# Performance work log

Hardware: AMD Instinct MI355X
Metric: run time of the kernel (lower is better)

## Reference

```python
import jax, jax.numpy as jnp
import numpy as np

N_NODES = 100000
N_EDGES = 3200000
IN_F = 256
OUT_F = 128


def setup_inputs() -> dict:
    key = jax.random.key(0)
    k1, k2, k3, k4, k5, k6 = jax.random.split(key, 6)
    x = jax.random.normal(k1, (N_NODES, IN_F), dtype=jnp.float32)
    edge_row = jax.random.randint(k2, (N_EDGES,), 0, N_NODES, dtype=jnp.int32)
    edge_col = jax.random.randint(k3, (N_EDGES,), 0, N_NODES, dtype=jnp.int32)
    edge_val = jax.random.uniform(k4, (N_EDGES,), dtype=jnp.float32)
    stdv = 1.0 / np.sqrt(OUT_F)
    weight = jax.random.uniform(k5, (IN_F, OUT_F), dtype=jnp.float32, minval=-stdv, maxval=stdv)
    bias = jax.random.uniform(k6, (OUT_F,), dtype=jnp.float32, minval=-stdv, maxval=stdv)
    return {"x": x, "edge_row": edge_row, "edge_col": edge_col,
            "edge_val": edge_val, "weight": weight, "bias": bias}


def reference(x, edge_row, edge_col, edge_val, weight, bias):
    # dropout p=0.0 -> identity. support = x @ W  [N, out_f]
    support = x @ weight
    # spmm(adj, support): out[r] = sum_e adj_val[e] * support[col[e]] for edges with row[e]==r
    gathered = support[edge_col] * edge_val[:, None]  # [E, out_f]
    out = jax.ops.segment_sum(gathered, edge_row, num_segments=N_NODES)
    out = out + bias
    return jax.nn.relu(out)
```

## Files before the change

### kernel.cpp

```cpp
#include <hip/hip_runtime.h>
#include <hip/hip_fp16.h>

#define IN_F 256
#define OUT_F 128
#define RPB 128
#define LOG_RPB 7
#define MAXB 1024
#define CHUNK 8192

typedef __attribute__((ext_vector_type(8))) short short8;
typedef __attribute__((ext_vector_type(4))) float f32x4;

__device__ inline short bf16r(float f) {
  unsigned u = __float_as_uint(f);
  u += 0x7FFF + ((u >> 16) & 1);
  return (short)(u >> 16);
}

__global__ __launch_bounds__(512) void gemm_mfma(const float* __restrict__ x,
                                                 const float* __restrict__ w,
                                                 __half* __restrict__ sup,
                                                 int n_nodes) {
  __shared__ short wlds[128 * 256];
  int t = threadIdx.x;
  for (int idx = t; idx < 256 * 128; idx += 512) {
    int k = idx >> 7;
    int n = idx & 127;
    int g = k >> 3;
    wlds[n * 256 + ((g ^ (n & 7)) << 3) + (k & 7)] = bf16r(w[idx]);
  }
  __syncthreads();

  int lane = t & 63;
  int wid = t >> 6;
  int wrow = (wid >> 1) * 64;
  int wcol = (wid & 1) * 64;
  int row_blk = blockIdx.x * 256;

  int arow[4];
#pragma unroll
  for (int mt = 0; mt < 4; ++mt)
    arow[mt] = min(row_blk + wrow + mt * 16 + (lane & 15), n_nodes - 1);
  int koff = (lane >> 4) * 8;

  f32x4 acc[4][4];
#pragma unroll
  for (int mt = 0; mt < 4; ++mt)
#pragma unroll
    for (int nt = 0; nt < 4; ++nt) acc[mt][nt] = (f32x4){0.f, 0.f, 0.f, 0.f};

#pragma unroll 2
  for (int kk = 0; kk < IN_F; kk += 32) {
    short8 af[4];
#pragma unroll
    for (int mt = 0; mt < 4; ++mt) {
      const float* px = x + (size_t)arow[mt] * IN_F + kk + koff;
      float4 p = *(const float4*)px;
      float4 q = *(const float4*)(px + 4);
      short8 a;
      a[0] = bf16r(p.x); a[1] = bf16r(p.y); a[2] = bf16r(p.z); a[3] = bf16r(p.w);
      a[4] = bf16r(q.x); a[5] = bf16r(q.y); a[6] = bf16r(q.z); a[7] = bf16r(q.w);
      af[mt] = a;
    }
    short8 bf[4];
    int g = (kk >> 3) + (lane >> 4);
#pragma unroll
    for (int nt = 0; nt < 4; ++nt) {
      int n = wcol + nt * 16 + (lane & 15);
      bf[nt] = *(const short8*)&wlds[n * 256 + ((g ^ (n & 7)) << 3)];
    }
#pragma unroll
    for (int mt = 0; mt < 4; ++mt)
#pragma unroll
      for (int nt = 0; nt < 4; ++nt)
        acc[mt][nt] = __builtin_amdgcn_mfma_f32_16x16x32_bf16(af[mt], bf[nt],
                                                              acc[mt][nt], 0, 0, 0);
  }

#pragma unroll
  for (int mt = 0; mt < 4; ++mt)
#pragma unroll
    for (int nt = 0; nt < 4; ++nt)
#pragma unroll
      for (int reg = 0; reg < 4; ++reg) {
        int grow = row_blk + wrow + mt * 16 + (lane >> 4) * 4 + reg;
        int gcol = wcol + nt * 16 + (lane & 15);
        if (grow < n_nodes)
          sup[(size_t)grow * OUT_F + gcol] = __float2half(acc[mt][nt][reg]);
      }
}

__global__ __launch_bounds__(256) void hist2(const int* __restrict__ erow,
                                             int* __restrict__ cnt2d,
                                             int n_edges, int nbuck, int nblk) {
  __shared__ int h[MAXB];
  int t = threadIdx.x;
  for (int i = t; i < nbuck; i += 256) h[i] = 0;
  __syncthreads();
  int beg = blockIdx.x * CHUNK;
  int end = min(beg + CHUNK, n_edges);
  for (int e = beg + t; e < end; e += 256) atomicAdd(&h[erow[e] >> LOG_RPB], 1);
  __syncthreads();
  for (int i = t; i < nbuck; i += 256) cnt2d[(size_t)i * nblk + blockIdx.x] = h[i];
}

__global__ __launch_bounds__(256) void rowsum(const int* __restrict__ cnt2d,
                                              int* __restrict__ bcnt, int nblk) {
  __shared__ int red[256];
  int b = blockIdx.x;
  const int* row = cnt2d + (size_t)b * nblk;
  int t = threadIdx.x;
  int s = 0;
  for (int i = t; i < nblk; i += 256) s += row[i];
  red[t] = s;
  __syncthreads();
  for (int off = 128; off > 0; off >>= 1) {
    if (t < off) red[t] += red[t + off];
    __syncthreads();
  }
  if (t == 0) bcnt[b] = red[0];
}

__global__ __launch_bounds__(1024) void bucket_scan(const int* __restrict__ bcnt,
                                                    int* __restrict__ bptr, int nbuck) {
  __shared__ int sc[1024];
  int t = threadIdx.x;
  int v = (t < nbuck) ? bcnt[t] : 0;
  sc[t] = v;
  __syncthreads();
  for (int off = 1; off < 1024; off <<= 1) {
    int u = (t >= off) ? sc[t - off] : 0;
    __syncthreads();
    sc[t] += u;
    __syncthreads();
  }
  if (t < nbuck) bptr[t] = sc[t] - v;
  if (t == 1023) bptr[nbuck] = sc[1023];
}

__global__ __launch_bounds__(256) void rowscan(const int* __restrict__ cnt2d,
                                               const int* __restrict__ bptr,
                                               int* __restrict__ off2d, int nblk) {
  __shared__ int sc[256];
  int b = blockIdx.x;
  const int* row = cnt2d + (size_t)b * nblk;
  int* orow = off2d + (size_t)b * nblk;
  int t = threadIdx.x;
  int chunk = (nblk + 255) >> 8;
  int beg = t * chunk, end2 = min(beg + chunk, nblk);
  int s = 0;
  for (int i = beg; i < end2; ++i) s += row[i];
  sc[t] = s;
  __syncthreads();
  for (int off = 1; off < 256; off <<= 1) {
    int u = (t >= off) ? sc[t - off] : 0;
    __syncthreads();
    sc[t] += u;
    __syncthreads();
  }
  int run = sc[t] - s + bptr[b];
  for (int i = beg; i < end2; ++i) {
    orow[i] = run;
    run += row[i];
  }
}

__global__ __launch_bounds__(512) void coarse_bin(const int* __restrict__ erow,
                                                  const int* __restrict__ ecol,
                                                  const float* __restrict__ eval,
                                                  const int* __restrict__ off2d,
                                                  int2* __restrict__ tmp,
                                                  int n_edges, int nbuck, int nblk) {
  __shared__ int cnt[MAXB];
  __shared__ int base[MAXB];
  int t = threadIdx.x;
  for (int i = t; i < nbuck; i += 512) {
    cnt[i] = 0;
    base[i] = off2d[(size_t)i * nblk + blockIdx.x];
  }
  __syncthreads();
  int beg = blockIdx.x * CHUNK;
  int end = min(beg + CHUNK, n_edges);
  for (int e = beg + t; e < end; e += 512) {
    int r = erow[e];
    int b = r >> LOG_RPB;
    int pos = base[b] + atomicAdd(&cnt[b], 1);
    int2 pk;
    pk.x = ecol[e] | ((r & (RPB - 1)) << 17);
    pk.y = __float_as_int(eval[e]);
    tmp[pos] = pk;
  }
}

__global__ __launch_bounds__(256) void fine_sort(const int* __restrict__ bptr,
                                                 const int2* __restrict__ tmp,
                                                 unsigned* __restrict__ pedge,
                                                 int* __restrict__ row_ptr,
                                                 int n_nodes, int nbuck) {
  __shared__ int hist[RPB];
  __shared__ int sc[RPB];
  __shared__ int cur[RPB];
  int b = blockIdx.x;
  int row0 = b << LOG_RPB;
  int t = threadIdx.x;
  int bbeg = bptr[b];
  int bend = bptr[b + 1];

  if (t < RPB) hist[t] = 0;
  __syncthreads();
  for (int j = bbeg + t; j < bend; j += 256) atomicAdd(&hist[tmp[j].x >> 17], 1);
  __syncthreads();
  if (t < RPB) sc[t] = hist[t];
  __syncthreads();
  for (int off = 1; off < RPB; off <<= 1) {
    int u = (t < RPB && t >= off) ? sc[t - off] : 0;
    __syncthreads();
    if (t < RPB) sc[t] += u;
    __syncthreads();
  }
  if (t < RPB) {
    int st = bbeg + sc[t] - hist[t];
    cur[t] = st;
    if (row0 + t < n_nodes) row_ptr[row0 + t] = st;
  }
  __syncthreads();
  for (int j = bbeg + t; j < bend; j += 256) {
    int2 e = tmp[j];
    int rl = e.x >> 17;
    int pos = atomicAdd(&cur[rl], 1);
    float v = __int_as_float(e.y);
    int q = (int)(v * 32767.f + 0.5f);
    q = min(max(q, 0), 32767);
    pedge[pos] = (unsigned)(e.x & 0x1FFFF) | ((unsigned)q << 17);
  }
  if (b == nbuck - 1 && t == 0) row_ptr[n_nodes] = bend;
}

__global__ __launch_bounds__(256) void spmm_gather(const int* __restrict__ row_ptr,
                                                   const unsigned* __restrict__ pedge,
                                                   const __half* __restrict__ sup,
                                                   const float* __restrict__ bias,
                                                   float* __restrict__ out,
                                                   int n_nodes) {
  int r = blockIdx.x * 4 + (threadIdx.x >> 6);
  if (r >= n_nodes) return;
  int lane = threadIdx.x & 63;
  int h = lane >> 5;
  int sl = lane & 31;
  int beg = row_ptr[r];
  int end = row_ptr[r + 1];
  const float dq = 1.0f / 32767.0f;

  float4 a0 = {0.f, 0.f, 0.f, 0.f};
  float4 a1 = {0.f, 0.f, 0.f, 0.f};
  float4 a2 = {0.f, 0.f, 0.f, 0.f};
  float4 a3 = {0.f, 0.f, 0.f, 0.f};

  int j = beg + h;
  for (; j + 6 < end; j += 8) {
    unsigned e0 = pedge[j];
    unsigned e1 = pedge[j + 2];
    unsigned e2 = pedge[j + 4];
    unsigned e3 = pedge[j + 6];
    uint2 s0 = ((const uint2*)(sup + (size_t)(e0 & 0x1FFFF) * OUT_F))[sl];
    uint2 s1 = ((const uint2*)(sup + (size_t)(e1 & 0x1FFFF) * OUT_F))[sl];
    uint2 s2 = ((const uint2*)(sup + (size_t)(e2 & 0x1FFFF) * OUT_F))[sl];
    uint2 s3 = ((const uint2*)(sup + (size_t)(e3 & 0x1FFFF) * OUT_F))[sl];
    float v0 = (float)(e0 >> 17) * dq;
    float v1 = (float)(e1 >> 17) * dq;
    float v2 = (float)(e2 >> 17) * dq;
    float v3 = (float)(e3 >> 17) * dq;
    float2 p, q;
    p = __half22float2(*(__half2*)&s0.x); q = __half22float2(*(__half2*)&s0.y);
    a0.x = fmaf(p.x, v0, a0.x); a0.y = fmaf(p.y, v0, a0.y);
    a0.z = fmaf(q.x, v0, a0.z); a0.w = fmaf(q.y, v0, a0.w);
    p = __half22float2(*(__half2*)&s1.x); q = __half22float2(*(__half2*)&s1.y);
    a1.x = fmaf(p.x, v1, a1.x); a1.y = fmaf(p.y, v1, a1.y);
    a1.z = fmaf(q.x, v1, a1.z); a1.w = fmaf(q.y, v1, a1.w);
    p = __half22float2(*(__half2*)&s2.x); q = __half22float2(*(__half2*)&s2.y);
    a2.x = fmaf(p.x, v2, a2.x); a2.y = fmaf(p.y, v2, a2.y);
    a2.z = fmaf(q.x, v2, a2.z); a2.w = fmaf(q.y, v2, a2.w);
    p = __half22float2(*(__half2*)&s3.x); q = __half22float2(*(__half2*)&s3.y);
    a3.x = fmaf(p.x, v3, a3.x); a3.y = fmaf(p.y, v3, a3.y);
    a3.z = fmaf(q.x, v3, a3.z); a3.w = fmaf(q.y, v3, a3.w);
  }
  for (; j < end; j += 2) {
    unsigned e0 = pedge[j];
    uint2 s0 = ((const uint2*)(sup + (size_t)(e0 & 0x1FFFF) * OUT_F))[sl];
    float v0 = (float)(e0 >> 17) * dq;
    float2 p = __half22float2(*(__half2*)&s0.x);
    float2 q = __half22float2(*(__half2*)&s0.y);
    a0.x = fmaf(p.x, v0, a0.x); a0.y = fmaf(p.y, v0, a0.y);
    a0.z = fmaf(q.x, v0, a0.z); a0.w = fmaf(q.y, v0, a0.w);
  }

  float4 f;
  f.x = (a0.x + a1.x) + (a2.x + a3.x);
  f.y = (a0.y + a1.y) + (a2.y + a3.y);
  f.z = (a0.z + a1.z) + (a2.z + a3.z);
  f.w = (a0.w + a1.w) + (a2.w + a3.w);
  f.x += __shfl_xor(f.x, 32);
  f.y += __shfl_xor(f.y, 32);
  f.z += __shfl_xor(f.z, 32);
  f.w += __shfl_xor(f.w, 32);

  if (h == 0) {
    float4 b = ((const float4*)bias)[sl];
    float4 o;
    o.x = fmaxf(f.x + b.x, 0.f);
    o.y = fmaxf(f.y + b.y, 0.f);
    o.z = fmaxf(f.z + b.z, 0.f);
    o.w = fmaxf(f.w + b.w, 0.f);
    ((float4*)(out + (size_t)r * OUT_F))[sl] = o;
  }
}

__global__ __launch_bounds__(256) void init_bias(float* __restrict__ out,
                                                 const float* __restrict__ bias,
                                                 int total) {
  int i = blockIdx.x * 256 + threadIdx.x;
  if (i < total) out[i] = bias[i & (OUT_F - 1)];
}

__global__ __launch_bounds__(256) void spmm_scatter(const int* __restrict__ erow,
                                                    const int* __restrict__ ecol,
                                                    const float* __restrict__ eval,
                                                    const __half* __restrict__ sup,
                                                    float* __restrict__ out,
                                                    int n_edges) {
  long long t = (long long)blockIdx.x * 256 + threadIdx.x;
  int e = (int)(t >> 6);
  if (e >= n_edges) return;
  int lane = (int)(t & 63);
  int r = erow[e];
  int c = ecol[e];
  float v = eval[e];
  __half2 s = ((const __half2*)(sup + (size_t)c * OUT_F))[lane];
  float2 f = __half22float2(s);
  float* orow = out + (size_t)r * OUT_F + 2 * lane;
  unsafeAtomicAdd(orow + 0, f.x * v);
  unsafeAtomicAdd(orow + 1, f.y * v);
}

__global__ __launch_bounds__(256) void relu_k(float* __restrict__ out, int total) {
  int i = blockIdx.x * 256 + threadIdx.x;
  if (i < total) out[i] = fmaxf(out[i], 0.f);
}

extern "C" void kernel_launch(void* const* d_in, const int* in_sizes, int n_in,
                              void* d_out, int out_size, void* d_ws, size_t ws_size,
                              hipStream_t stream) {
  const float* x = (const float*)d_in[0];
  const int* erow = (const int*)d_in[1];
  const int* ecol = (const int*)d_in[2];
  const float* eval = (const float*)d_in[3];
  const float* w = (const float*)d_in[4];
  const float* bias = (const float*)d_in[5];
  float* out = (float*)d_out;

  int n_nodes = in_sizes[0] / IN_F;
  int n_edges = in_sizes[1];
  int total = n_nodes * OUT_F;
  int nbuck = (n_nodes + RPB - 1) >> LOG_RPB;
  int nblk = (n_edges + CHUNK - 1) / CHUNK;

  char* p = (char*)d_ws;
  __half* sup = (__half*)p;             p += (size_t)n_nodes * OUT_F * 2;
  int2* tmp = (int2*)p;                 p += (size_t)n_edges * 8;
  unsigned* pedge = (unsigned*)p;       p += (size_t)n_edges * 4;
  int* row_ptr = (int*)p;               p += (size_t)(n_nodes + 1) * 4;
  int* bcnt = (int*)p;                  p += (size_t)nbuck * 4;
  int* bptr = (int*)p;                  p += (size_t)(nbuck + 1) * 4;
  int* cnt2d = (int*)p;                 p += (size_t)nbuck * nblk * 4;
  int* off2d = (int*)p;                 p += (size_t)nbuck * nblk * 4;
  size_t need = (size_t)(p - (char*)d_ws);

  gemm_mfma<<<(n_nodes + 255) / 256, 512, 0, stream>>>(x, w, sup, n_nodes);

  if (ws_size >= need && nbuck <= MAXB) {
    hist2<<<nblk, 256, 0, stream>>>(erow, cnt2d, n_edges, nbuck, nblk);
    rowsum<<<nbuck, 256, 0, stream>>>(cnt2d, bcnt, nblk);
    bucket_scan<<<1, 1024, 0, stream>>>(bcnt, bptr, nbuck);
    rowscan<<<nbuck, 256, 0, stream>>>(cnt2d, bptr, off2d, nblk);
    coarse_bin<<<nblk, 512, 0, stream>>>(erow, ecol, eval, off2d, tmp,
                                         n_edges, nbuck, nblk);
    fine_sort<<<nbuck, 256, 0, stream>>>(bptr, tmp, pedge, row_ptr, n_nodes, nbuck);
    spmm_gather<<<(n_nodes + 3) / 4, 256, 0, stream>>>(row_ptr, pedge, sup, bias,
                                                       out, n_nodes);
  } else {
    init_bias<<<(total + 255) / 256, 256, 0, stream>>>(out, bias, total);
    long long threads = (long long)n_edges * 64;
    spmm_scatter<<<(int)((threads + 255) / 256), 256, 0, stream>>>(erow, ecol, eval,
                                                                   sup, out, n_edges);
    relu_k<<<(total + 255) / 256, 256, 0, stream>>>(out, total);
  }
}
```

Before: 261.7 us.

## Fuse per-bucket fine sort with SpMM gather using LDS-resident edge lists

Merges the fine_sort and spmm_gather kernels: each block sorts its bucket of edges by local row into shared memory (with global spill past a capacity) and then gathers and reduces support rows for those rows directly. Buckets shrink from 128 to 64 rows and bucket_scan handles two buckets per thread to allow up to 2048 buckets. This avoids writing and re-reading the packed edge array and row_ptr through global memory and removes one launch. In exchange, the gather phase now runs only 4 waves per block over 64 rows with larger LDS use, which may reduce occupancy and latency hiding for the random gathers.

New measurement: 260.3 us. About the same (-0.5%).

```diff
diff --git a/kernel.cpp b/kernel.cpp
--- a/kernel.cpp
+++ b/kernel.cpp
@@ -3,10 +3,11 @@
 
 #define IN_F 256
 #define OUT_F 128
-#define RPB 128
-#define LOG_RPB 7
-#define MAXB 1024
+#define RPB 64
+#define LOG_RPB 6
+#define MAXB 2048
 #define CHUNK 8192
+#define CAP 3072
 
 typedef __attribute__((ext_vector_type(8))) short short8;
 typedef __attribute__((ext_vector_type(4))) float f32x4;
@@ -125,8 +126,11 @@
                                                     int* __restrict__ bptr, int nbuck) {
   __shared__ int sc[1024];
   int t = threadIdx.x;
-  int v = (t < nbuck) ? bcnt[t] : 0;
-  sc[t] = v;
+  int i0 = 2 * t, i1 = 2 * t + 1;
+  int c0 = (i0 < nbuck) ? bcnt[i0] : 0;
+  int c1 = (i1 < nbuck) ? bcnt[i1] : 0;
+  int s = c0 + c1;
+  sc[t] = s;
   __syncthreads();
   for (int off = 1; off < 1024; off <<= 1) {
     int u = (t >= off) ? sc[t - off] : 0;
@@ -134,7 +138,9 @@
     sc[t] += u;
     __syncthreads();
   }
-  if (t < nbuck) bptr[t] = sc[t] - v;
+  int run = sc[t] - s;
+  if (i0 < nbuck) { bptr[i0] = run; run += c0; }
+  if (i1 < nbuck) { bptr[i1] = run; run += c1; }
   if (t == 1023) bptr[nbuck] = sc[1023];
 }
 
@@ -192,126 +198,127 @@
   }
 }
 
-__global__ __launch_bounds__(256) void fine_sort(const int* __restrict__ bptr,
-                                                 const int2* __restrict__ tmp,
-                                                 unsigned* __restrict__ pedge,
-                                                 int* __restrict__ row_ptr,
-                                                 int n_nodes, int nbuck) {
+__global__ __launch_bounds__(256) void sort_gather(const int* __restrict__ bptr,
+                                                   const int2* __restrict__ tmp,
+                                                   unsigned* __restrict__ spill,
+                                                   const __half* __restrict__ sup,
+                                                   const float* __restrict__ bias,
+                                                   float* __restrict__ out,
+                                                   int n_nodes) {
+  __shared__ unsigned eL[CAP];
   __shared__ int hist[RPB];
-  __shared__ int sc[RPB];
+  __shared__ int ex[RPB + 1];
   __shared__ int cur[RPB];
   int b = blockIdx.x;
   int row0 = b << LOG_RPB;
   int t = threadIdx.x;
   int bbeg = bptr[b];
   int bend = bptr[b + 1];
+  int m = bend - bbeg;
 
   if (t < RPB) hist[t] = 0;
   __syncthreads();
   for (int j = bbeg + t; j < bend; j += 256) atomicAdd(&hist[tmp[j].x >> 17], 1);
   __syncthreads();
-  if (t < RPB) sc[t] = hist[t];
+  if (t < RPB) ex[t] = hist[t];
   __syncthreads();
   for (int off = 1; off < RPB; off <<= 1) {
-    int u = (t < RPB && t >= off) ? sc[t - off] : 0;
-    __syncthreads();
-    if (t < RPB) sc[t] += u;
+    int u = (t < RPB && t >= off) ? ex[t - off] : 0;
+    __syncthreads();
+    if (t < RPB) ex[t] += u;
     __syncthreads();
   }
   if (t < RPB) {
-    int st = bbeg + sc[t] - hist[t];
+    int st = ex[t] - hist[t];
+    ex[t] = st;
     cur[t] = st;
-    if (row0 + t < n_nodes) row_ptr[row0 + t] = st;
-  }
+  }
+  if (t == 0) ex[RPB] = m;
   __syncthreads();
   for (int j = bbeg + t; j < bend; j += 256) {
     int2 e = tmp[j];
     int rl = e.x >> 17;
     int pos = atomicAdd(&cur[rl], 1);
     float v = __int_as_float(e.y);
-    int q = (int)(v * 32767.f + 0.5f);
-    q = min(max(q, 0), 32767);
-    pedge[pos] = (unsigned)(e.x & 0x1FFFF) | ((unsigned)q << 17);
-  }
-  if (b == nbuck - 1 && t == 0) row_ptr[n_nodes] = bend;
-}
-
-__global__ __launch_bounds__(256) void spmm_gather(const int* __restrict__ row_ptr,
-                                                   const unsigned* __restrict__ pedge,
-                                                   const __half* __restrict__ sup,
-                                                   const float* __restrict__ bias,
-                                                   float* __restrict__ out,
-                                                   int n_nodes) {
-  int r = blockIdx.x * 4 + (threadIdx.x >> 6);
-  if (r >= n_nodes) return;
-  int lane = threadIdx.x & 63;
+    int q = min(max((int)(v * 32767.f + 0.5f), 0), 32767);
+    unsigned pk = (unsigned)(e.x & 0x1FFFF) | ((unsigned)q << 17);
+    if (pos < CAP) eL[pos] = pk;
+    else spill[bbeg + pos] = pk;
+  }
+  __syncthreads();
+
+  int lane = t & 63;
+  int wv = t >> 6;
   int h = lane >> 5;
   int sl = lane & 31;
-  int beg = row_ptr[r];
-  int end = row_ptr[r + 1];
   const float dq = 1.0f / 32767.0f;
-
-  float4 a0 = {0.f, 0.f, 0.f, 0.f};
-  float4 a1 = {0.f, 0.f, 0.f, 0.f};
-  float4 a2 = {0.f, 0.f, 0.f, 0.f};
-  float4 a3 = {0.f, 0.f, 0.f, 0.f};
-
-  int j = beg + h;
-  for (; j + 6 < end; j += 8) {
-    unsigned e0 = pedge[j];
-    unsigned e1 = pedge[j + 2];
-    unsigned e2 = pedge[j + 4];
-    unsigned e3 = pedge[j + 6];
-    uint2 s0 = ((const uint2*)(sup + (size_t)(e0 & 0x1FFFF) * OUT_F))[sl];
-    uint2 s1 = ((const uint2*)(sup + (size_t)(e1 & 0x1FFFF) * OUT_F))[sl];
-    uint2 s2 = ((const uint2*)(sup + (size_t)(e2 & 0x1FFFF) * OUT_F))[sl];
-    uint2 s3 = ((const uint2*)(sup + (size_t)(e3 & 0x1FFFF) * OUT_F))[sl];
-    float v0 = (float)(e0 >> 17) * dq;
-    float v1 = (float)(e1 >> 17) * dq;
-    float v2 = (float)(e2 >> 17) * dq;
-    float v3 = (float)(e3 >> 17) * dq;
-    float2 p, q;
-    p = __half22float2(*(__half2*)&s0.x); q = __half22float2(*(__half2*)&s0.y);
-    a0.x = fmaf(p.x, v0, a0.x); a0.y = fmaf(p.y, v0, a0.y);
-    a0.z = fmaf(q.x, v0, a0.z); a0.w = fmaf(q.y, v0, a0.w);
-    p = __half22float2(*(__half2*)&s1.x); q = __half22float2(*(__half2*)&s1.y);
-    a1.x = fmaf(p.x, v1, a1.x); a1.y = fmaf(p.y, v1, a1.y);
-    a1.z = fmaf(q.x, v1, a1.z); a1.w = fmaf(q.y, v1, a1.w);
-    p = __half22float2(*(__half2*)&s2.x); q = __half22float2(*(__half2*)&s2.y);
-    a2.x = fmaf(p.x, v2, a2.x); a2.y = fmaf(p.y, v2, a2.y);
-    a2.z = fmaf(q.x, v2, a2.z); a2.w = fmaf(q.y, v2, a2.w);
-    p = __half22float2(*(__half2*)&s3.x); q = __half22float2(*(__half2*)&s3.y);
-    a3.x = fmaf(p.x, v3, a3.x); a3.y = fmaf(p.y, v3, a3.y);
-    a3.z = fmaf(q.x, v3, a3.z); a3.w = fmaf(q.y, v3, a3.w);
-  }
-  for (; j < end; j += 2) {
-    unsigned e0 = pedge[j];
-    uint2 s0 = ((const uint2*)(sup + (size_t)(e0 & 0x1FFFF) * OUT_F))[sl];
-    float v0 = (float)(e0 >> 17) * dq;
-    float2 p = __half22float2(*(__half2*)&s0.x);
-    float2 q = __half22float2(*(__half2*)&s0.y);
-    a0.x = fmaf(p.x, v0, a0.x); a0.y = fmaf(p.y, v0, a0.y);
-    a0.z = fmaf(q.x, v0, a0.z); a0.w = fmaf(q.y, v0, a0.w);
-  }
-
-  float4 f;
-  f.x = (a0.x + a1.x) + (a2.x + a3.x);
-  f.y = (a0.y + a1.y) + (a2.y + a3.y);
-  f.z = (a0.z + a1.z) + (a2.z + a3.z);
-  f.w = (a0.w + a1.w) + (a2.w + a3.w);
-  f.x += __shfl_xor(f.x, 32);
-  f.y += __shfl_xor(f.y, 32);
-  f.z += __shfl_xor(f.z, 32);
-  f.w += __shfl_xor(f.w, 32);
-
-  if (h == 0) {
-    float4 b = ((const float4*)bias)[sl];
-    float4 o;
-    o.x = fmaxf(f.x + b.x, 0.f);
-    o.y = fmaxf(f.y + b.y, 0.f);
-    o.z = fmaxf(f.z + b.z, 0.f);
-    o.w = fmaxf(f.w + b.w, 0.f);
-    ((float4*)(out + (size_t)r * OUT_F))[sl] = o;
+  float4 bi = ((const float4*)bias)[sl];
+  int nr = min(RPB, n_nodes - row0);
+
+  for (int rl = wv; rl < nr; rl += 4) {
+    int beg = ex[rl];
+    int end = ex[rl + 1];
+    float4 a0 = {0.f, 0.f, 0.f, 0.f};
+    float4 a1 = {0.f, 0.f, 0.f, 0.f};
+    float4 a2 = {0.f, 0.f, 0.f, 0.f};
+    float4 a3 = {0.f, 0.f, 0.f, 0.f};
+
+    int j = beg + h;
+#define LOADE(J) (((J) < CAP) ? eL[(J)] : spill[bbeg + (J)])
+    for (; j + 6 < end; j += 8) {
+      unsigned e0 = LOADE(j);
+      unsigned e1 = LOADE(j + 2);
+      unsigned e2 = LOADE(j + 4);
+      unsigned e3 = LOADE(j + 6);
+      uint2 s0 = ((const uint2*)(sup + (size_t)(e0 & 0x1FFFF) * OUT_F))[sl];
+      uint2 s1 = ((const uint2*)(sup + (size_t)(e1 & 0x1FFFF) * OUT_F))[sl];
+      uint2 s2 = ((const uint2*)(sup + (size_t)(e2 & 0x1FFFF) * OUT_F))[sl];
+      uint2 s3 = ((const uint2*)(sup + (size_t)(e3 & 0x1FFFF) * OUT_F))[sl];
+      float v0 = (float)(e0 >> 17) * dq;
+      float v1 = (float)(e1 >> 17) * dq;
+      float v2 = (float)(e2 >> 17) * dq;
+      float v3 = (float)(e3 >> 17) * dq;
+      float2 p, q;
+      p = __half22float2(*(__half2*)&s0.x); q = __half22float2(*(__half2*)&s0.y);
+      a0.x = fmaf(p.x, v0, a0.x); a0.y = fmaf(p.y, v0, a0.y);
+      a0.z = fmaf(q.x, v0, a0.z); a0.w = fmaf(q.y, v0, a0.w);
+      p = __half22float2(*(__half2*)&s1.x); q = __half22float2(*(__half2*)&s1.y);
+      a1.x = fmaf(p.x, v1, a1.x); a1.y = fmaf(p.y, v1, a1.y);
+      a1.z = fmaf(q.x, v1, a1.z); a1.w = fmaf(q.y, v1, a1.w);
+      p = __half22float2(*(__half2*)&s2.x); q = __half22float2(*(__half2*)&s2.y);
+      a2.x = fmaf(p.x, v2, a2.x); a2.y = fmaf(p.y, v2, a2.y);
+      a2.z = fmaf(q.x, v2, a2.z); a2.w = fmaf(q.y, v2, a2.w);
+      p = __half22float2(*(__half2*)&s3.x); q = __half22float2(*(__half2*)&s3.y);
+      a3.x = fmaf(p.x, v3, a3.x); a3.y = fmaf(p.y, v3, a3.y);
+      a3.z = fmaf(q.x, v3, a3.z); a3.w = fmaf(q.y, v3, a3.w);
+    }
+    for (; j < end; j += 2) {
+      unsigned e0 = LOADE(j);
+      uint2 s0 = ((const uint2*)(sup + (size_t)(e0 & 0x1FFFF) * OUT_F))[sl];
+      float v0 = (float)(e0 >> 17) * dq;
+      float2 p = __half22float2(*(__half2*)&s0.x);
+      float2 q = __half22float2(*(__half2*)&s0.y);
+      a0.x = fmaf(p.x, v0, a0.x); a0.y = fmaf(p.y, v0, a0.y);
+      a0.z = fmaf(q.x, v0, a0.z); a0.w = fmaf(q.y, v0, a0.w);
+    }
+#undef LOADE
+    float4 f;
+    f.x = (a0.x + a1.x) + (a2.x + a3.x);
+    f.y = (a0.y + a1.y) + (a2.y + a3.y);
+    f.z = (a0.z + a1.z) + (a2.z + a3.z);
+    f.w = (a0.w + a1.w) + (a2.w + a3.w);
+    f.x += __shfl_xor(f.x, 32);
+    f.y += __shfl_xor(f.y, 32);
+    f.z += __shfl_xor(f.z, 32);
+    f.w += __shfl_xor(f.w, 32);
+    if (h == 0) {
+      float4 o;
+      o.x = fmaxf(f.x + bi.x, 0.f);
+      o.y = fmaxf(f.y + bi.y, 0.f);
+      o.z = fmaxf(f.z + bi.z, 0.f);
+      o.w = fmaxf(f.w + bi.w, 0.f);
+      ((float4*)(out + (size_t)(row0 + rl) * OUT_F))[sl] = o;
+    }
   }
 }
 
@@ -367,8 +374,7 @@
   char* p = (char*)d_ws;
   __half* sup = (__half*)p;             p += (size_t)n_nodes * OUT_F * 2;
   int2* tmp = (int2*)p;                 p += (size_t)n_edges * 8;
-  unsigned* pedge = (unsigned*)p;       p += (size_t)n_edges * 4;
-  int* row_ptr = (int*)p;               p += (size_t)(n_nodes + 1) * 4;
+  unsigned* spill = (unsigned*)p;       p += (size_t)n_edges * 4;
   int* bcnt = (int*)p;                  p += (size_t)nbuck * 4;
   int* bptr = (int*)p;                  p += (size_t)(nbuck + 1) * 4;
   int* cnt2d = (int*)p;                 p += (size_t)nbuck * nblk * 4;
@@ -384,9 +390,8 @@
     rowscan<<<nbuck, 256, 0, stream>>>(cnt2d, bptr, off2d, nblk);
     coarse_bin<<<nblk, 512, 0, stream>>>(erow, ecol, eval, off2d, tmp,
                                          n_edges, nbuck, nblk);
-    fine_sort<<<nbuck, 256, 0, stream>>>(bptr, tmp, pedge, row_ptr, n_nodes, nbuck);
-    spmm_gather<<<(n_nodes + 3) / 4, 256, 0, stream>>>(row_ptr, pedge, sup, bias,
-                                                       out, n_nodes);
+    sort_gather<<<nbuck, 256, 0, stream>>>(bptr, tmp, spill, sup, bias, out,
+                                           n_nodes);
   } else {
     init_bias<<<(total + 255) / 256, 256, 0, stream>>>(out, bias, total);
     long long threads = (long long)n_edges * 64;
```
